# Performance work log

Hardware: AMD Instinct MI355X
Metric: run time of the kernel (lower is better)

The kernel has to match this reference:

```python
import jax, jax.numpy as jnp
import numpy as np
from jax import lax

EPS_BN = 1e-5
EPS_NORM = 1e-12
D = 6                      # max_displacement
K = 2 * D + 1              # 13

def _conv(x, w, b, stride=1, pad=0):
    out = lax.conv_general_dilated(x, w, (stride, stride), [(pad, pad), (pad, pad)],
                                   dimension_numbers=('NCHW', 'OIHW', 'NCHW'))
    return out + b[None, :, None, None]

def _bn(x, g, be):
    m = x.mean(axis=(0, 2, 3), keepdims=True)
    v = x.var(axis=(0, 2, 3), keepdims=True)  # biased var, as torch BN uses for normalization
    return g[None, :, None, None] * (x - m) * lax.rsqrt(v + EPS_BN) + be[None, :, None, None]

def _lrelu(x):
    return jax.nn.leaky_relu(x, 0.1)

def _encoder(x, w1, b1, g1, be1, w2, b2, g2, be2, w3, b3, g3, be3):
    fine = _lrelu(_bn(_conv(x, w1, b1, pad=3), g1, be1))          # (B,16,64,64)
    h = _lrelu(_bn(_conv(fine, w2, b2, stride=2, pad=2), g2, be2))  # (B,32,32,32)
    coarse = _lrelu(_bn(_conv(h, w3, b3, pad=1), g3, be3))        # (B,32,32,32)
    return coarse, fine

def _l2norm_c(f):
    n = jnp.sqrt(jnp.sum(f * f, axis=1, keepdims=True))
    return f / jnp.maximum(n, EPS_NORM)

def _correlation(fA, fB):
    # cost[b, i*K+j, h, w] = sum_c fA_n[b,c,h,w] * fB_n_pad[b,c,h+i,w+j]
    B, C, H, W = fA.shape
    fA = _l2norm_c(fA)
    fB = _l2norm_c(fB)
    fBp = jnp.pad(fB, ((0, 0), (0, 0), (D, D), (D, D)))
    costs = []
    for i in range(K):          # small fixed displacement set (169 slices)
        for j in range(K):
            costs.append(jnp.sum(fA * fBp[:, :, i:i + H, j:j + W], axis=1))
    return jnp.stack(costs, axis=1)  # (B, K*K, H, W), matches unfold ordering

def _decoder(cost, skipA, skipB, wc1, bc1, wc2, bc2, wf1, bf1, wf2, bf2, wo, bo):
    x = _lrelu(_conv(cost, wc1, bc1, pad=1))
    x = _lrelu(_conv(x, wc2, bc2, pad=1))        # (B,64,32,32)
    x = jnp.repeat(jnp.repeat(x, 2, axis=2), 2, axis=3)
    x = jnp.concatenate([x, skipA, skipB], axis=1)       # (B,96,64,64)
    x = _lrelu(_conv(x, wf1, bf1, pad=1))
    x = _lrelu(_conv(x, wf2, bf2, pad=1))        # (B,32,64,64)
    return _conv(x, wo, bo, pad=0)               # (B,2,64,64)

def setup_inputs() -> dict:
    key = jax.random.key(0)
    ks = jax.random.split(key, 16)
    B = 32
    n_disp = K * K  # 169
    f32 = jnp.float32
    w = lambda k, shp: (jax.random.normal(k, shp, dtype=f32) * 0.05)
    inp = {
        'frameA': jax.random.normal(ks[0], (B, 1, 64, 64), dtype=f32),
        'frameB': jax.random.normal(ks[1], (B, 1, 64, 64), dtype=f32),
        # shared siamese encoder params
        'w1': w(ks[2], (16, 1, 7, 7)),  'b1': jnp.zeros((16,), f32),
        'g1': jnp.ones((16,), f32),     'be1': jnp.zeros((16,), f32),
        'w2': w(ks[3], (32, 16, 5, 5)), 'b2': jnp.zeros((32,), f32),
        'g2': jnp.ones((32,), f32),     'be2': jnp.zeros((32,), f32),
        'w3': w(ks[4], (32, 32, 3, 3)), 'b3': jnp.zeros((32,), f32),
        'g3': jnp.ones((32,), f32),     'be3': jnp.zeros((32,), f32),
        # decoder params
        'wc1': w(ks[5], (128, n_disp, 3, 3)), 'bc1': jnp.zeros((128,), f32),
        'wc2': w(ks[6], (64, 128, 3, 3)),     'bc2': jnp.zeros((64,), f32),
        'wf1': w(ks[7], (64, 96, 3, 3)),      'bf1': jnp.zeros((64,), f32),
        'wf2': w(ks[8], (32, 64, 3, 3)),      'bf2': jnp.zeros((32,), f32),
        'wo':  w(ks[9], (2, 32, 1, 1)),       'bo': jnp.zeros((2,), f32),
    }
    return inp

def reference(frameA, frameB, w1, b1, g1, be1, w2, b2, g2, be2, w3, b3, g3, be3,
              wc1, bc1, wc2, bc2, wf1, bf1, wf2, bf2, wo, bo):
    coarseA, skipA = _encoder(frameA, w1, b1, g1, be1, w2, b2, g2, be2, w3, b3, g3, be3)
    coarseB, skipB = _encoder(frameB, w1, b1, g1, be1, w2, b2, g2, be2, w3, b3, g3, be3)
    cost = _correlation(coarseA, coarseB)
    return _decoder(cost, skipA, skipB, wc1, bc1, wc2, bc2, wf1, bf1, wf2, bf2, wo, bo)
```

## Files before the change

kernel.cpp:

```cpp
#include <hip/hip_runtime.h>

typedef __attribute__((ext_vector_type(4))) float f32x4;
typedef __attribute__((ext_vector_type(8))) short bf16x8;

#define BN_EPS 1e-5f
constexpr int BATCH = 32;

static inline int cdiv(int a, int b) { return (a + b - 1) / b; }

__device__ __forceinline__ float lrelu(float v) { return v > 0.f ? v : 0.1f * v; }

__device__ __forceinline__ unsigned short f2bf(float f) {
    unsigned u = __float_as_uint(f);
    u = (u + 0x7FFFu + ((u >> 16) & 1u)) >> 16;
    return (unsigned short)u;
}
__device__ __forceinline__ float bf2f(unsigned short s) {
    return __uint_as_float(((unsigned)s) << 16);
}

#define SWZ(e)  ((e) ^ ((((e) >> 6) & 3) << 3))
#define FSWZ(e) ((e) ^ ((((e) >> 5) & 7) << 2))

__global__ void prep_w_all(const float* w1, const float* w2, const float* w3, const float* w4,
                           const float* wE2s, const float* wE3s,
                           unsigned short* d1, unsigned short* d2, unsigned short* d3,
                           unsigned short* d4, unsigned short* dE2, unsigned short* dE3)
{
    int idx = blockIdx.x * blockDim.x + threadIdx.x;
    if (idx < 368640) {
        const float* src; unsigned short* dst; int COUT, CINS, CINP;
        if (idx < 221184)      { src = w1; dst = d1; COUT = 128; CINS = 169; CINP = 192; }
        else if (idx < 294912) { src = w2; dst = d2; COUT = 64;  CINS = 128; CINP = 128; idx -= 221184; }
        else if (idx < 350208) { src = w3; dst = d3; COUT = 64;  CINS = 96;  CINP = 96;  idx -= 294912; }
        else                   { src = w4; dst = d4; COUT = 32;  CINS = 64;  CINP = 64;  idx -= 350208; }
        int ic  = idx % CINP;
        int oc  = (idx / CINP) % COUT;
        int tap = idx / (CINP * COUT);
        float v = (ic < CINS) ? src[((size_t)oc * CINS + ic) * 9 + tap] : 0.f;
        dst[((size_t)tap * COUT + oc) * CINP + ic] = f2bf(v);
    } else if (idx < 381952) {
        idx -= 368640;
        int c = idx % 32, oc = (idx / 32) % 32, s = idx / 1024;
        int tap = 2 * s + (c >= 16 ? 1 : 0);
        int ic = c & 15;
        float v = (tap < 25) ? wE2s[((size_t)oc * 16 + ic) * 25 + tap] : 0.f;
        dE2[idx] = f2bf(v);
    } else if (idx < 391168) {
        idx -= 381952;
        int ic = idx % 32, oc = (idx / 32) % 32, tap = idx / 1024;
        dE3[idx] = f2bf(wE3s[((size_t)oc * 32 + ic) * 9 + tap]);
    }
}

template<int CIN, int COUT, int H, int TH, int MODE, int OM>
__global__ __launch_bounds__(256) void conv3x3_mfma(
    const unsigned short* __restrict__ in,
    const unsigned short* __restrict__ in2,
    const unsigned short* __restrict__ wT,
    const float* __restrict__ bias,
    unsigned short* __restrict__ out,
    float* __restrict__ dout,
    const float* __restrict__ w1x1,
    const float* __restrict__ b1x1)
{
    constexpr int MB = (COUT >= 64) ? 64 : COUT;
    constexpr int MFRAGS = MB / 16;
    constexpr int WM = 2;
    constexpr int MW = MFRAGS / WM;
    constexpr int NW = 4 / MW;
    constexpr int WN = TH / NW;

    __shared__ unsigned short s_w[9 * MB * 32];
    __shared__ unsigned short s_in[(TH + 2) * 18 * 32];

    const int tid  = threadIdx.x;
    const int wid  = tid >> 6;
    const int lane = tid & 63;
    const int l15  = lane & 15;
    const int kg   = lane >> 4;
    constexpr int TILESX = H / 16;
    const int bx = blockIdx.x;
    const int x0 = (bx % TILESX) * 16;
    const int y0 = (bx / TILESX) * TH;
    const int ocbase = blockIdx.y * MB;
    const int n = blockIdx.z;

    const int mw = wid % MW;
    const int nw = wid / MW;

    f32x4 acc[WM][WN];
    #pragma unroll
    for (int i = 0; i < WM; ++i) {
        #pragma unroll
        for (int r = 0; r < 4; ++r) {
            float bv = bias[ocbase + (mw * WM + i) * 16 + kg * 4 + r];
            #pragma unroll
            for (int j = 0; j < WN; ++j) acc[i][j][r] = bv;
        }
    }

    for (int c0 = 0; c0 < CIN; c0 += 32) {
        for (int t = tid; t < 9 * MB * 4; t += 256) {
            int sub = t & 3;
            int row = t >> 2;
            int tap = row / MB, oc = row % MB;
            const unsigned short* src = wT + ((size_t)(tap * COUT + ocbase + oc) * CIN + c0) + sub * 8;
            *(int4*)&s_w[SWZ(row * 32 + sub * 8)] = *(const int4*)src;
        }
        for (int t = tid; t < (TH + 2) * 18 * 4; t += 256) {
            int sub = t & 3;
            int p = t >> 2;
            int y = p / 18, x = p - y * 18;
            int gy = y0 - 1 + y, gx = x0 - 1 + x;
            int4 v = {0, 0, 0, 0};
            if ((unsigned)gy < (unsigned)H && (unsigned)gx < (unsigned)H) {
                if (MODE == 0) {
                    v = *(const int4*)&in[((size_t)(n * H + gy) * H + gx) * CIN + c0 + sub * 8];
                } else {
                    if (c0 < 64) {
                        v = *(const int4*)&in[((size_t)(n * 32 + (gy >> 1)) * 32 + (gx >> 1)) * 64 + c0 + sub * 8];
                    } else {
                        int f  = sub >> 1;
                        int cc = (sub & 1) * 8;
                        v = *(const int4*)&in2[((size_t)((f * BATCH + n) * 64 + gy) * 64 + gx) * 16 + cc];
                    }
                }
            }
            *(int4*)&s_in[SWZ(p * 32 + sub * 8)] = v;
        }
        __syncthreads();

        #pragma unroll
        for (int tap = 0; tap < 9; ++tap) {
            const int kh = tap / 3, kw = tap - (tap / 3) * 3;
            bf16x8 a[WM], b[WN];
            #pragma unroll
            for (int i = 0; i < WM; ++i) {
                int mf = mw * WM + i;
                a[i] = *(const bf16x8*)&s_w[SWZ((tap * MB + mf * 16 + l15) * 32 + kg * 8)];
            }
            #pragma unroll
            for (int j = 0; j < WN; ++j) {
                int nf = nw * WN + j;
                b[j] = *(const bf16x8*)&s_in[SWZ(((nf + kh) * 18 + l15 + kw) * 32 + kg * 8)];
            }
            #pragma unroll
            for (int i = 0; i < WM; ++i)
                #pragma unroll
                for (int j = 0; j < WN; ++j)
                    acc[i][j] = __builtin_amdgcn_mfma_f32_16x16x32_bf16(a[i], b[j], acc[i][j], 0, 0, 0);
        }
        __syncthreads();
    }

    if constexpr (OM == 2) {
        __shared__ unsigned short sC[16 * 16 * 32];
        #pragma unroll
// ... 19 lines not shown
            int c = q * 4;
            float x0v = bf2f(v.x), x1v = bf2f(v.y), x2v = bf2f(v.z), x3v = bf2f(v.w);
            a0 = fmaf(x0v, w1x1[c], a0);     a1 = fmaf(x0v, w1x1[32 + c], a1);
            a0 = fmaf(x1v, w1x1[c + 1], a0); a1 = fmaf(x1v, w1x1[32 + c + 1], a1);
            a0 = fmaf(x2v, w1x1[c + 2], a0); a1 = fmaf(x2v, w1x1[32 + c + 2], a1);
            a0 = fmaf(x3v, w1x1[c + 3], a0); a1 = fmaf(x3v, w1x1[32 + c + 3], a1);
        }
        int row = tid >> 4, col = tid & 15;
        int gy = y0 + row, gx = x0 + col;
        dout[((size_t)n * 2) * 4096 + gy * 64 + gx]     = a0;
        dout[((size_t)n * 2 + 1) * 4096 + gy * 64 + gx] = a1;
    } else {
        #pragma unroll
        for (int i = 0; i < WM; ++i) {
            int oc = ocbase + (mw * WM + i) * 16 + kg * 4;
            #pragma unroll
            for (int j = 0; j < WN; ++j) {
                int nf = nw * WN + j;
                int gy = y0 + nf, gx = x0 + l15;
                size_t base = ((size_t)(n * H + gy) * H + gx) * COUT + oc;
                if (OM == 0) {
                    ushort4 pk;
                    pk.x = f2bf(lrelu(acc[i][j][0]));
                    pk.y = f2bf(lrelu(acc[i][j][1]));
                    pk.z = f2bf(lrelu(acc[i][j][2]));
                    pk.w = f2bf(lrelu(acc[i][j][3]));
                    *(ushort4*)&out[base] = pk;
                } else {
                    *(f32x4*)&((float*)out)[base] = acc[i][j];
                }
            }
        }
    }
}

__global__ __launch_bounds__(256) void conv2s_mfma(
    const unsigned short* __restrict__ in, const unsigned short* __restrict__ wS,
    const float* __restrict__ bias, unsigned short* __restrict__ outN,
    float2* __restrict__ part)
{
    __shared__ unsigned short s_w[13 * 32 * 32];
    __shared__ unsigned short s_in[20 * 36 * 16];
    __shared__ float2 redC[4][4][8];

    const int tid = threadIdx.x;
    const int nw  = tid >> 6;
    const int lane = tid & 63;
    const int l15 = lane & 15;
    const int kg  = lane >> 4;
    const int x0 = (blockIdx.x & 1) * 16;
    const int y0 = (blockIdx.x >> 1) * 8;
    const int n  = blockIdx.z;

    f32x4 acc[2][2];
    #pragma unroll
    for (int i = 0; i < 2; ++i) {
        #pragma unroll
        for (int r = 0; r < 4; ++r) {
            float bv = bias[i * 16 + kg * 4 + r];
            acc[i][0][r] = bv; acc[i][1][r] = bv;
        }
    }

    for (int t = tid; t < 1664; t += 256) {
        int sub = t & 3, row = t >> 2;
        *(int4*)&s_w[SWZ(row * 32 + sub * 8)] = *(const int4*)&wS[row * 32 + sub * 8];
    }
    for (int t = tid; t < 1440; t += 256) {
        int sub = t & 1, p = t >> 1;
        int y = p / 36, x = p - y * 36;
        int gy = 2 * y0 - 2 + y, gx = 2 * x0 - 2 + x;
        int4 v = {0, 0, 0, 0};
        if ((unsigned)gy < 64u && (unsigned)gx < 64u)
            v = *(const int4*)&in[((size_t)(n * 64 + gy) * 64 + gx) * 16 + sub * 8];
        *(int4*)&s_in[SWZ((y * 36 + x) * 16 + sub * 8)] = v;
    }
    __syncthreads();

    #pragma unroll
    for (int s = 0; s < 13; ++s) {
        int tA = 2 * s, tB = 2 * s + 1;
        int khA = tA / 5, kwA = tA % 5;
        int khB = tB / 5, kwB = tB % 5;
        int kh = (kg < 2) ? khA : khB;
        int kw = (kg < 2) ? kwA : kwB;
        int co = (kg & 1) * 8;
        bf16x8 a[2], b[2];
        a[0] = *(const bf16x8*)&s_w[SWZ((s * 32 + l15) * 32 + kg * 8)];
        a[1] = *(const bf16x8*)&s_w[SWZ((s * 32 + 16 + l15) * 32 + kg * 8)];
        #pragma unroll
        for (int j = 0; j < 2; ++j) {
            int py = nw * 2 + j;
            b[j] = *(const bf16x8*)&s_in[SWZ(((2 * py + kh) * 36 + 2 * l15 + kw) * 16 + co)];
        }
        acc[0][0] = __builtin_amdgcn_mfma_f32_16x16x32_bf16(a[0], b[0], acc[0][0], 0, 0, 0);
        acc[0][1] = __builtin_amdgcn_mfma_f32_16x16x32_bf16(a[0], b[1], acc[0][1], 0, 0, 0);
        acc[1][0] = __builtin_amdgcn_mfma_f32_16x16x32_bf16(a[1], b[0], acc[1][0], 0, 0, 0);
        acc[1][1] = __builtin_amdgcn_mfma_f32_16x16x32_bf16(a[1], b[1], acc[1][1], 0, 0, 0);
    }

    #pragma unroll
    for (int i = 0; i < 2; ++i)
        #pragma unroll
        for (int j = 0; j < 2; ++j) {
            int gy = y0 + nw * 2 + j, gx = x0 + l15;
            ushort4 pk;
            pk.x = f2bf(acc[i][j][0]); pk.y = f2bf(acc[i][j][1]);
// ... 2 lines not shown
        }

    float t1[2][4], t2[2][4];
    #pragma unroll
    for (int i = 0; i < 2; ++i)
        #pragma unroll
        for (int r = 0; r < 4; ++r) {
            float v0 = acc[i][0][r], v1 = acc[i][1][r];
            t1[i][r] = v0 + v1;
            t2[i][r] = v0 * v0 + v1 * v1;
        }
    #pragma unroll
    for (int off = 8; off > 0; off >>= 1)
        #pragma unroll
        for (int i = 0; i < 2; ++i)
            #pragma unroll
            for (int r = 0; r < 4; ++r) {
                t1[i][r] += __shfl_down(t1[i][r], off);
                t2[i][r] += __shfl_down(t2[i][r], off);
            }
    if (l15 == 0) {
        #pragma unroll
        for (int i = 0; i < 2; ++i)
            #pragma unroll
            for (int r = 0; r < 4; ++r)
                redC[nw][kg][i * 4 + r] = make_float2(t1[i][r], t2[i][r]);
    }
    __syncthreads();
    if (tid < 32) {
        int oc = tid;
        int i = oc >> 4, kq = (oc & 15) >> 2, r = oc & 3;
        float2 s = redC[0][kq][i * 4 + r];
        #pragma unroll
        for (int w = 1; w < 4; ++w) {
            float2 p = redC[w][kq][i * 4 + r];
            s.x += p.x; s.y += p.y;
        }
        int f = n >> 5, slot = blockIdx.x * 32 + (n & 31);
        part[(size_t)(f * 32 + oc) * 256 + slot] = s;
    }
}

__global__ __launch_bounds__(256) void conv1_tiled(
    const float* __restrict__ fA, const float* __restrict__ fB,
    const float* __restrict__ w, const float* __restrict__ bias,
    unsigned short* __restrict__ outN, float2* __restrict__ part)
{
    __shared__ float s_in[38][40];
    __shared__ float s_w[49][8];
    __shared__ float2 red1[4][8];

    const int tid = threadIdx.x;
    const int tx = tid & 15, ty = tid >> 4;
    const int tile = blockIdx.x;
    const int x0 = (tile & 1) << 5;
    const int y0 = (tile >> 1) << 5;
    const int ocbase = blockIdx.y * 8;
    const int n = blockIdx.z;
    const float* in = (n < BATCH) ? (fA + (size_t)n * 4096) : (fB + (size_t)(n - BATCH) * 4096);

    for (int t = tid; t < 49 * 8; t += 256) {
        int oc = t & 7, k = t >> 3;
        s_w[k][oc] = w[(ocbase + oc) * 49 + k];
    }
    for (int t = tid; t < 38 * 38; t += 256) {
        int y = t / 38, x = t - (t / 38) * 38;
        int gy = y0 + y - 3, gx = x0 + x - 3;
        float v = 0.f;
        if ((unsigned)gy < 64u && (unsigned)gx < 64u) v = in[gy * 64 + gx];
        s_in[y][x] = v;
    }
    __syncthreads();

    float acc[8][4];
    #pragma unroll
    for (int oc = 0; oc < 8; ++oc) {
        float bv = bias[ocbase + oc];
        acc[oc][0] = bv; acc[oc][1] = bv; acc[oc][2] = bv; acc[oc][3] = bv;
    }
    #pragma unroll
    for (int kh = 0; kh < 7; ++kh) {
        #pragma unroll
        for (int kw = 0; kw < 7; ++kw) {
            float i00 = s_in[ty + kh][tx + kw];
            float i01 = s_in[ty + kh][tx + 16 + kw];
            float i10 = s_in[ty + 16 + kh][tx + kw];
            float i11 = s_in[ty + 16 + kh][tx + 16 + kw];
            #pragma unroll
            for (int oc = 0; oc < 8; ++oc) {
                float wv = s_w[kh * 7 + kw][oc];
                acc[oc][0] = fmaf(i00, wv, acc[oc][0]);
                acc[oc][1] = fmaf(i01, wv, acc[oc][1]);
                acc[oc][2] = fmaf(i10, wv, acc[oc][2]);
                acc[oc][3] = fmaf(i11, wv, acc[oc][3]);
            }
        }
    }
    #pragma unroll
    for (int i = 0; i < 2; ++i)
        #pragma unroll
        for (int j = 0; j < 2; ++j) {
            int k = i * 2 + j;
            int oy = y0 + ty + i * 16, ox = x0 + tx + j * 16;
            ushort4 p0, p1;
            p0.x = f2bf(acc[0][k]); p0.y = f2bf(acc[1][k]);
            p0.z = f2bf(acc[2][k]); p0.w = f2bf(acc[3][k]);
            p1.x = f2bf(acc[4][k]); p1.y = f2bf(acc[5][k]);
            p1.z = f2bf(acc[6][k]); p1.w = f2bf(acc[7][k]);
            unsigned short* dst = outN + ((size_t)n * 4096 + oy * 64 + ox) * 16 + ocbase;
            *(ushort4*)dst = p0;
            *(ushort4*)(dst + 4) = p1;
        }
    float v1[8], v2[8];
    #pragma unroll
    for (int oc = 0; oc < 8; ++oc) {
        v1[oc] = acc[oc][0] + acc[oc][1] + acc[oc][2] + acc[oc][3];
        v2[oc] = acc[oc][0] * acc[oc][0] + acc[oc][1] * acc[oc][1]
               + acc[oc][2] * acc[oc][2] + acc[oc][3] * acc[oc][3];
    }
    #pragma unroll
    for (int off = 32; off > 0; off >>= 1)
        #pragma unroll
        for (int oc = 0; oc < 8; ++oc) {
            v1[oc] += __shfl_down(v1[oc], off);
            v2[oc] += __shfl_down(v2[oc], off);
        }
    int wid = tid >> 6, lane = tid & 63;
    if (lane == 0)
        #pragma unroll
        for (int oc = 0; oc < 8; ++oc) red1[wid][oc] = make_float2(v1[oc], v2[oc]);
    __syncthreads();
    if (tid < 8) {
        float2 s = red1[0][tid];
        #pragma unroll
        for (int w2_ = 1; w2_ < 4; ++w2_) { s.x += red1[w2_][tid].x; s.y += red1[w2_][tid].y; }
        int f = n >> 5, slot = blockIdx.x * 32 + (n & 31);
        part[(size_t)(f * 16 + ocbase + tid) * 128 + slot] = s;
    }
}

template<int C, int NS>
__global__ void bn_part_nhwc(const float* __restrict__ x, float2* __restrict__ part, int HW)
{
    constexpr int G = 256 / C;
    int f = blockIdx.x / NS, s = blockIdx.x % NS;
    int RS = (32 * HW) / NS;
    const float* base = x + ((size_t)f * 32 * HW + (size_t)s * RS) * C;
    int c = threadIdx.x % C, rg = threadIdx.x / C;
    float s1 = 0.f, s2 = 0.f;
    for (int r = rg; r < RS; r += G) {
        float v = base[(size_t)r * C + c];
        s1 += v; s2 += v * v;
    }
    __shared__ float2 sh[256];
    sh[threadIdx.x] = make_float2(s1, s2);
    __syncthreads();
    for (int off = 128; off >= C; off >>= 1) {
        if (threadIdx.x < off) {
            float2 o = sh[threadIdx.x + off];
            sh[threadIdx.x].x += o.x; sh[threadIdx.x].y += o.y;
        }
        __syncthreads();
    }
    if (threadIdx.x < C) part[(size_t)(f * C + c) * NS + s] = sh[threadIdx.x];
}

template<int C, int NS>
__device__ __forceinline__ void finalize_stats(const float2* __restrict__ part, int f,
                                               float inv, float* sstats)
{
    __shared__ float2 red[256];
    int t = threadIdx.x;
    int c = t % C, k = t / C;
    float s1 = 0.f, s2 = 0.f;
    for (int q = k; q < NS; q += 256 / C) {
        float2 p = part[(size_t)(f * C + c) * NS + q];
        s1 += p.x; s2 += p.y;
    }
    red[t] = make_float2(s1, s2);
    __syncthreads();
    for (int off = 128; off >= C; off >>= 1) {
        if (t < off) { red[t].x += red[t + off].x; red[t].y += red[t + off].y; }
        __syncthreads();
    }
    if (t < C) {
        float m = red[t].x * inv;
        float var = red[t].y * inv - m * m;
        sstats[2 * t]     = m;
        sstats[2 * t + 1] = rsqrtf(var + BN_EPS);
    }
    __syncthreads();
}

__global__ __launch_bounds__(256) void bn1_apply(unsigned short* __restrict__ xN,
                          const float2* __restrict__ part,
                          const float* __restrict__ g, const float* __restrict__ be)
{
    __shared__ float sst[32];
    int idx = blockIdx.x * blockDim.x + threadIdx.x;
    int f = idx >> 17;
    finalize_stats<16, 128>(part, f, 1.f / (32.f * 4096.f), sst);
    unsigned short* p = xN + (size_t)idx * 16;
    int4 v0 = *(int4*)p, v1 = *(int4*)(p + 8);
    unsigned short* s = (unsigned short*)&v0;
    unsigned short o[16];
    #pragma unroll
    for (int c = 0; c < 8; ++c)
        o[c] = f2bf(lrelu((bf2f(s[c]) - sst[2 * c]) * sst[2 * c + 1] * g[c] + be[c]));
    s = (unsigned short*)&v1;
    #pragma unroll
    for (int c = 0; c < 8; ++c)
        o[8 + c] = f2bf(lrelu((bf2f(s[c]) - sst[2 * (8 + c)]) * sst[2 * (8 + c) + 1] * g[8 + c] + be[8 + c]));
    *(int4*)p       = *(int4*)&o[0];
    *(int4*)(p + 8) = *(int4*)&o[8];
}

__global__ __launch_bounds__(256) void bn2_apply(unsigned short* __restrict__ xN,
                          const float2* __restrict__ part,
                          const float* __restrict__ g, const float* __restrict__ be)
{
    __shared__ float sst[64];
    int idx = blockIdx.x * blockDim.x + threadIdx.x;
    int f = idx >> 15;
    finalize_stats<32, 256>(part, f, 1.f / (32.f * 1024.f), sst);
    unsigned short* p = xN + (size_t)idx * 32;
    unsigned short o[32];
    #pragma unroll
    for (int q = 0; q < 4; ++q) {
        int4 v = *(int4*)(p + q * 8);
        unsigned short* s = (unsigned short*)&v;
        #pragma unroll
        for (int k = 0; k < 8; ++k) {
            int c = q * 8 + k;
            o[c] = f2bf(lrelu((bf2f(s[k]) - sst[2 * c]) * sst[2 * c + 1] * g[c] + be[c]));
        }
    }
    #pragma unroll
    for (int q = 0; q < 4; ++q) *(int4*)(p + q * 8) = *(int4*)&o[q * 8];
}

__global__ __launch_bounds__(256) void bn3_l2n_nhwc(const float* __restrict__ xN,
                             const float2* __restrict__ part,
                             const float* __restrict__ g, const float* __restrict__ be,
                             float* __restrict__ outN)
{
    __shared__ float sst[64];
    int idx = blockIdx.x * blockDim.x + threadIdx.x;
    int f = idx >> 15;
    finalize_stats<32, 128>(part, f, 1.f / (32.f * 1024.f), sst);
    const float* src = xN + (size_t)idx * 32;
    float v[32];
    float ss = 0.f;
    #pragma unroll
    for (int c = 0; c < 32; ++c) {
        float t = lrelu((src[c] - sst[2 * c]) * sst[2 * c + 1] * g[c] + be[c]);
        v[c] = t; ss += t * t;
    }
    float inv = 1.f / fmaxf(sqrtf(ss), 1e-12f);
    float* dst = outN + (size_t)idx * 32;
    #pragma unroll
    for (int c = 0; c < 32; ++c) dst[c] = v[c] * inv;
}

#define CSWZ(c, w) ((c) ^ (((w) & 7) << 2))

__global__ __launch_bounds__(256) void corr_tile(const float* __restrict__ xN,
                                                 unsigned short* __restrict__ cost)
{
    __shared__ float sA[32 * 32];
    __shared__ float sB[13][32 * 32];
    __shared__ unsigned short sC[32][176];

    const int h = blockIdx.x, b = blockIdx.y;
    const float* Ab = xN + ((size_t)b * 1024 + h * 32) * 32;
    const float* Bb = xN + ((size_t)(BATCH + b) * 1024) * 32;

    {
        int t = threadIdx.x;
        int w = t >> 3, gr = t & 7;
        f32x4 v = *(const f32x4*)&Ab[w * 32 + gr * 4];
        *(f32x4*)&sA[w * 32 + CSWZ(gr * 4, w)] = v;
    }
    for (int t = threadIdx.x; t < 13 * 256; t += 256) {
        int row = t >> 8, q = t & 255;
        int w = q >> 3, gr = q & 7;
        int gh = h + row - 6;
        f32x4 v = {0.f, 0.f, 0.f, 0.f};
        if ((unsigned)gh < 32u) v = *(const f32x4*)&Bb[((size_t)gh * 32 + w) * 32 + gr * 4];
        *(f32x4*)&sB[row][w * 32 + CSWZ(gr * 4, w)] = v;
    }
    __syncthreads();

    const int w = threadIdx.x & 31;
    const int g = threadIdx.x >> 5;
    f32x4 a[8];
    #pragma unroll
    for (int gr = 0; gr < 8; ++gr) a[gr] = *(const f32x4*)&sA[w * 32 + CSWZ(gr * 4, w)];

    for (int dy = g; dy < 13; dy += 8) {
        #pragma unroll
        for (int dx = 0; dx < 13; ++dx) {
            int wb = w + dx - 6;
            float s = 0.f;
            if ((unsigned)wb < 32u) {
                #pragma unroll
                for (int gr = 0; gr < 8; ++gr) {
                    f32x4 bv = *(const f32x4*)&sB[dy][wb * 32 + CSWZ(gr * 4, wb)];
                    s += a[gr].x * bv.x + a[gr].y * bv.y + a[gr].z * bv.z + a[gr].w * bv.w;
                }
            }
            sC[w][dy * 13 + dx] = f2bf(s);
        }
    }
    __syncthreads();

    for (int t = threadIdx.x; t < 32 * 169; t += 256) {
        int ww = t / 169;
        int d  = t - ww * 169;
        cost[((size_t)(b * 1024) + h * 32 + ww) * 192 + d] = sC[ww][d];
    }
}

extern "C" void kernel_launch(void* const* d_in, const int* in_sizes, int n_in,
                              void* d_out, int out_size, void* d_ws, size_t ws_size,
                              hipStream_t stream)
{
    const float* frameA = (const float*)d_in[0];
    const float* frameB = (const float*)d_in[1];
    const float* w1  = (const float*)d_in[2];
    const float* b1  = (const float*)d_in[3];
    const float* g1  = (const float*)d_in[4];
    const float* be1 = (const float*)d_in[5];
    const float* w2  = (const float*)d_in[6];
    const float* b2  = (const float*)d_in[7];
    const float* g2  = (const float*)d_in[8];
    const float* be2 = (const float*)d_in[9];
    const float* w3  = (const float*)d_in[10];
    const float* b3  = (const float*)d_in[11];
    const float* g3  = (const float*)d_in[12];
    const float* be3 = (const float*)d_in[13];
    const float* wc1 = (const float*)d_in[14];
    const float* bc1 = (const float*)d_in[15];
    const float* wc2 = (const float*)d_in[16];
    const float* bc2 = (const float*)d_in[17];
    const float* wf1 = (const float*)d_in[18];
    const float* bf1 = (const float*)d_in[19];
    const float* wf2 = (const float*)d_in[20];
    const float* bf2 = (const float*)d_in[21];
    const float* wo  = (const float*)d_in[22];
    const float* bo  = (const float*)d_in[23];

    float* ws      = (float*)d_ws;
    float* c3N     = ws;
    float* coarseN = c3N + 2097152;
    float2* part   = (float2*)(coarseN + 2097152);
    unsigned short* fineN = (unsigned short*)(part + 16384);
    unsigned short* h2bf  = fineN + 4194304;
    unsigned short* costN = h2bf + 2097152;
    unsigned short* d1    = costN + 6291456;
    unsigned short* d2    = d1 + 4194304;
    unsigned short* f1o   = d2 + 2097152;
    unsigned short* wT1   = f1o + 8388608;
    unsigned short* wT2   = wT1 + 221184;
    unsigned short* wTf1  = wT2 + 73728;
    unsigned short* wTf2  = wTf1 + 55296;
    unsigned short* wE2   = wTf2 + 18432;
    unsigned short* wE3   = wE2 + 13312;

    const int T = 256;

    prep_w_all<<<cdiv(391168, T), T, 0, stream>>>(wc1, wc2, wf1, wf2, w2, w3,
                                                  wT1, wT2, wTf1, wTf2, wE2, wE3);

    conv1_tiled<<<dim3(4, 2, 2 * BATCH), T, 0, stream>>>(frameA, frameB, w1, b1, fineN, part);
    bn1_apply<<<1024, T, 0, stream>>>(fineN, part, g1, be1);

    conv2s_mfma<<<dim3(8, 1, 64), T, 0, stream>>>(fineN, wE2, b2, h2bf, part);
    bn2_apply<<<256, T, 0, stream>>>(h2bf, part, g2, be2);

    conv3x3_mfma<32, 32, 32, 8, 0, 1><<<dim3(8, 1, 64), T, 0, stream>>>(
        h2bf, nullptr, wE3, b3, (unsigned short*)c3N, nullptr, nullptr, nullptr);
    bn_part_nhwc<32, 128><<<2 * 128, T, 0, stream>>>(c3N, part, 1024);
    bn3_l2n_nhwc<<<256, T, 0, stream>>>(c3N, part, g3, be3, coarseN);

    corr_tile<<<dim3(32, BATCH), T, 0, stream>>>(coarseN, costN);

    conv3x3_mfma<192, 128, 32, 8, 0, 0><<<dim3(8, 2, BATCH), T, 0, stream>>>(
        costN, nullptr, wT1, bc1, d1, nullptr, nullptr, nullptr);
    conv3x3_mfma<128, 64, 32, 8, 0, 0><<<dim3(8, 1, BATCH), T, 0, stream>>>(
        d1, nullptr, wT2, bc2, d2, nullptr, nullptr, nullptr);
    conv3x3_mfma<96, 64, 64, 8, 1, 0><<<dim3(32, 1, BATCH), T, 0, stream>>>(
        d2, fineN, wTf1, bf1, f1o, nullptr, nullptr, nullptr);
    conv3x3_mfma<64, 32, 64, 16, 0, 2><<<dim3(16, 1, BATCH), T, 0, stream>>>(
        f1o, nullptr, wTf2, bf2, nullptr, (float*)d_out, wo, bo);
}
```

Measured before the change: 198.7 us.

## Fuse BN apply and L2 norm into consumer kernels, merge weight prep with conv1

Drops the separate BN apply, BN partial-stat, and BN3+L2-norm kernels. Each consumer kernel now reduces the partial statistics itself and applies BN plus leaky ReLU while loading its input tile. The conv3 epilogue emits the per-channel partial sums, and the correlation kernel computes per-pixel L2 norms in shared memory and scales the dot products by them. Weight preparation now runs as extra blocks of the conv1 kernel, removing a launch. In exchange, every block repeats the stats finalization, and the fused conv tiles recompute BN on halo reads.

Result: slower. 222.7 us (+12.1%).

```diff
diff --git a/kernel.cpp b/kernel.cpp
--- a/kernel.cpp
+++ b/kernel.cpp
@@ -21,39 +21,167 @@
 
 #define SWZ(e)  ((e) ^ ((((e) >> 6) & 3) << 3))
 #define FSWZ(e) ((e) ^ ((((e) >> 5) & 7) << 2))
-
-__global__ void prep_w_all(const float* w1, const float* w2, const float* w3, const float* w4,
-                           const float* wE2s, const float* wE3s,
-                           unsigned short* d1, unsigned short* d2, unsigned short* d3,
-                           unsigned short* d4, unsigned short* dE2, unsigned short* dE3)
+#define CSWZ(c, w) ((c) ^ (((w) & 7) << 2))
+
+template<int C, int NS>
+__device__ __forceinline__ void finalize_stats(const float2* __restrict__ part, int f,
+                                               float inv, float* sstats)
 {
-    int idx = blockIdx.x * blockDim.x + threadIdx.x;
-    if (idx < 368640) {
-        const float* src; unsigned short* dst; int COUT, CINS, CINP;
-        if (idx < 221184)      { src = w1; dst = d1; COUT = 128; CINS = 169; CINP = 192; }
-        else if (idx < 294912) { src = w2; dst = d2; COUT = 64;  CINS = 128; CINP = 128; idx -= 221184; }
-        else if (idx < 350208) { src = w3; dst = d3; COUT = 64;  CINS = 96;  CINP = 96;  idx -= 294912; }
-        else                   { src = w4; dst = d4; COUT = 32;  CINS = 64;  CINP = 64;  idx -= 350208; }
-        int ic  = idx % CINP;
-        int oc  = (idx / CINP) % COUT;
-        int tap = idx / (CINP * COUT);
-        float v = (ic < CINS) ? src[((size_t)oc * CINS + ic) * 9 + tap] : 0.f;
-        dst[((size_t)tap * COUT + oc) * CINP + ic] = f2bf(v);
-    } else if (idx < 381952) {
-        idx -= 368640;
-        int c = idx % 32, oc = (idx / 32) % 32, s = idx / 1024;
-        int tap = 2 * s + (c >= 16 ? 1 : 0);
-        int ic = c & 15;
-        float v = (tap < 25) ? wE2s[((size_t)oc * 16 + ic) * 25 + tap] : 0.f;
-        dE2[idx] = f2bf(v);
-    } else if (idx < 391168) {
-        idx -= 381952;
-        int ic = idx % 32, oc = (idx / 32) % 32, tap = idx / 1024;
-        dE3[idx] = f2bf(wE3s[((size_t)oc * 32 + ic) * 9 + tap]);
-    }
+    __shared__ float2 red[256];
+    int t = threadIdx.x;
+    int c = t % C, k = t / C;
+    float s1 = 0.f, s2 = 0.f;
+    for (int q = k; q < NS; q += 256 / C) {
+        float2 p = part[(size_t)(f * C + c) * NS + q];
+        s1 += p.x; s2 += p.y;
+    }
+    red[t] = make_float2(s1, s2);
+    __syncthreads();
+    for (int off = 128; off >= C; off >>= 1) {
+        if (t < off) { red[t].x += red[t + off].x; red[t].y += red[t + off].y; }
+        __syncthreads();
+    }
+    if (t < C) {
+        float m = red[t].x * inv;
+        float var = red[t].y * inv - m * m;
+        sstats[2 * t]     = m;
+        sstats[2 * t + 1] = rsqrtf(var + BN_EPS);
+    }
+    __syncthreads();
 }
 
-template<int CIN, int COUT, int H, int TH, int MODE, int OM>
+__global__ __launch_bounds__(256) void conv1_prep(
+    const float* __restrict__ fA, const float* __restrict__ fB,
+    const float* __restrict__ w, const float* __restrict__ bias,
+    unsigned short* __restrict__ outN, float2* __restrict__ part1,
+    const float* wd1, const float* wd2, const float* wd3, const float* wd4,
+    const float* wE2s, const float* wE3s,
+    unsigned short* d1, unsigned short* d2, unsigned short* d3,
+    unsigned short* d4, unsigned short* dE2, unsigned short* dE3)
+{
+    const int gid = blockIdx.x;
+    if (gid >= 512) {
+        int idx = (gid - 512) * 256 + threadIdx.x;
+        if (idx < 368640) {
+            const float* src; unsigned short* dst; int COUT, CINS, CINP;
+            if (idx < 221184)      { src = wd1; dst = d1; COUT = 128; CINS = 169; CINP = 192; }
+            else if (idx < 294912) { src = wd2; dst = d2; COUT = 64;  CINS = 128; CINP = 128; idx -= 221184; }
+            else if (idx < 350208) { src = wd3; dst = d3; COUT = 64;  CINS = 96;  CINP = 96;  idx -= 294912; }
+            else                   { src = wd4; dst = d4; COUT = 32;  CINS = 64;  CINP = 64;  idx -= 350208; }
+            int ic  = idx % CINP;
+            int oc  = (idx / CINP) % COUT;
+            int tap = idx / (CINP * COUT);
+            float v = (ic < CINS) ? src[((size_t)oc * CINS + ic) * 9 + tap] : 0.f;
+            dst[((size_t)tap * COUT + oc) * CINP + ic] = f2bf(v);
+        } else if (idx < 381952) {
+            idx -= 368640;
+            int c = idx % 32, oc = (idx / 32) % 32, s = idx / 1024;
+            int tap = 2 * s + (c >= 16 ? 1 : 0);
+            int ic = c & 15;
+            float v = (tap < 25) ? wE2s[((size_t)oc * 16 + ic) * 25 + tap] : 0.f;
+            dE2[idx] = f2bf(v);
+        } else if (idx < 391168) {
+            idx -= 381952;
+            int ic = idx % 32, oc = (idx / 32) % 32, tap = idx / 1024;
+            dE3[idx] = f2bf(wE3s[((size_t)oc * 32 + ic) * 9 + tap]);
+        }
+        return;
+    }
+
+    __shared__ float s_in[38][40];
+    __shared__ float s_w[49][8];
+    __shared__ float2 red1[4][8];
+
+    const int tid = threadIdx.x;
+    const int tx = tid & 15, ty = tid >> 4;
+    const int tile = gid & 3;
+    const int ocbase = ((gid >> 2) & 1) * 8;
+    const int n = gid >> 3;
+    const int x0 = (tile & 1) << 5;
+    const int y0 = (tile >> 1) << 5;
+    const float* in = (n < BATCH) ? (fA + (size_t)n * 4096) : (fB + (size_t)(n - BATCH) * 4096);
+
+    for (int t = tid; t < 49 * 8; t += 256) {
+        int oc = t & 7, k = t >> 3;
+        s_w[k][oc] = w[(ocbase + oc) * 49 + k];
+    }
+    for (int t = tid; t < 38 * 38; t += 256) {
+        int y = t / 38, x = t - (t / 38) * 38;
+        int gy = y0 + y - 3, gx = x0 + x - 3;
+        float v = 0.f;
+        if ((unsigned)gy < 64u && (unsigned)gx < 64u) v = in[gy * 64 + gx];
+        s_in[y][x] = v;
+    }
+    __syncthreads();
+
+    float acc[8][4];
+    #pragma unroll
+    for (int oc = 0; oc < 8; ++oc) {
+        float bv = bias[ocbase + oc];
+        acc[oc][0] = bv; acc[oc][1] = bv; acc[oc][2] = bv; acc[oc][3] = bv;
+    }
+    #pragma unroll
+    for (int kh = 0; kh < 7; ++kh) {
+        #pragma unroll
+        for (int kw = 0; kw < 7; ++kw) {
+            float i00 = s_in[ty + kh][tx + kw];
+            float i01 = s_in[ty + kh][tx + 16 + kw];
+            float i10 = s_in[ty + 16 + kh][tx + kw];
+            float i11 = s_in[ty + 16 + kh][tx + 16 + kw];
+            #pragma unroll
+            for (int oc = 0; oc < 8; ++oc) {
+                float wv = s_w[kh * 7 + kw][oc];
+                acc[oc][0] = fmaf(i00, wv, acc[oc][0]);
+                acc[oc][1] = fmaf(i01, wv, acc[oc][1]);
+                acc[oc][2] = fmaf(i10, wv, acc[oc][2]);
+                acc[oc][3] = fmaf(i11, wv, acc[oc][3]);
+            }
+        }
+    }
+    #pragma unroll
+    for (int i = 0; i < 2; ++i)
+        #pragma unroll
+        for (int j = 0; j < 2; ++j) {
+            int k = i * 2 + j;
+            int oy = y0 + ty + i * 16, ox = x0 + tx + j * 16;
+            ushort4 p0, p1;
+            p0.x = f2bf(acc[0][k]); p0.y = f2bf(acc[1][k]);
+            p0.z = f2bf(acc[2][k]); p0.w = f2bf(acc[3][k]);
+            p1.x = f2bf(acc[4][k]); p1.y = f2bf(acc[5][k]);
+            p1.z = f2bf(acc[6][k]); p1.w = f2bf(acc[7][k]);
+            unsigned short* dst = outN + ((size_t)n * 4096 + oy * 64 + ox) * 16 + ocbase;
+            *(ushort4*)dst = p0;
+            *(ushort4*)(dst + 4) = p1;
+        }
+    float v1[8], v2[8];
+    #pragma unroll
+    for (int oc = 0; oc < 8; ++oc) {
+        v1[oc] = acc[oc][0] + acc[oc][1] + acc[oc][2] + acc[oc][3];
+        v2[oc] = acc[oc][0] * acc[oc][0] + acc[oc][1] * acc[oc][1]
+               + acc[oc][2] * acc[oc][2] + acc[oc][3] * acc[oc][3];
+    }
+    #pragma unroll
+    for (int off = 32; off > 0; off >>= 1)
+        #pragma unroll
+        for (int oc = 0; oc < 8; ++oc) {
+            v1[oc] += __shfl_down(v1[oc], off);
+            v2[oc] += __shfl_down(v2[oc], off);
+        }
+    int wid = tid >> 6, lane = tid & 63;
+    if (lane == 0)
+        #pragma unroll
+        for (int oc = 0; oc < 8; ++oc) red1[wid][oc] = make_float2(v1[oc], v2[oc]);
+    __syncthreads();
+    if (tid < 8) {
+        float2 s = red1[0][tid];
+        #pragma unroll
+        for (int q = 1; q < 4; ++q) { s.x += red1[q][tid].x; s.y += red1[q][tid].y; }
+        int f = n >> 5, slot = tile * 32 + (n & 31);
+        part1[(size_t)(f * 16 + ocbase + tid) * 128 + slot] = s;
+    }
+}
+
+template<int CIN, int COUT, int H, int TH, int MODE, int OM, int INBN>
 __global__ __launch_bounds__(256) void conv3x3_mfma(
     const unsigned short* __restrict__ in,
     const unsigned short* __restrict__ in2,
@@ -62,7 +190,11 @@
     unsigned short* __restrict__ out,
     float* __restrict__ dout,
     const float* __restrict__ w1x1,
-    const float* __restrict__ b1x1)
+    const float* __restrict__ b1x1,
+    const float2* __restrict__ partIn,
+    const float* __restrict__ gIn,
+    const float* __restrict__ beIn,
+    float2* __restrict__ partOut)
 {
     constexpr int MB = (COUT >= 64) ? 64 : COUT;
     constexpr int MFRAGS = MB / 16;
@@ -73,6 +205,7 @@
 
     __shared__ unsigned short s_w[9 * MB * 32];
     __shared__ unsigned short s_in[(TH + 2) * 18 * 32];
+    __shared__ float sstIn[64];
 
     const int tid  = threadIdx.x;
     const int wid  = tid >> 6;
@@ -89,6 +222,11 @@
     const int mw = wid % MW;
     const int nw = wid / MW;
 
+    if constexpr (INBN == 1)
+        finalize_stats<32, 128>(partIn, 0, 1.f / (32.f * 4096.f), sstIn);
+    if constexpr (INBN == 2)
+        finalize_stats<32, 256>(partIn, n >> 5, 1.f / (32.f * 1024.f), sstIn);
+
     f32x4 acc[WM][WN];
     #pragma unroll
     for (int i = 0; i < WM; ++i) {
@@ -117,6 +255,15 @@
             if ((unsigned)gy < (unsigned)H && (unsigned)gx < (unsigned)H) {
                 if (MODE == 0) {
                     v = *(const int4*)&in[((size_t)(n * H + gy) * H + gx) * CIN + c0 + sub * 8];
+                    if constexpr (INBN == 2) {
+                        unsigned short* e = (unsigned short*)&v;
+                        #pragma unroll
+                        for (int k = 0; k < 8; ++k) {
+                            int c = c0 + sub * 8 + k;
+                            float xv = bf2f(e[k]);
+                            e[k] = f2bf(lrelu((xv - sstIn[2 * c]) * sstIn[2 * c + 1] * gIn[c] + beIn[c]));
+                        }
+                    }
                 } else {
                     if (c0 < 64) {
                         v = *(const int4*)&in[((size_t)(n * 32 + (gy >> 1)) * 32 + (gx >> 1)) * 64 + c0 + sub * 8];
@@ -124,6 +271,16 @@
                         int f  = sub >> 1;
                         int cc = (sub & 1) * 8;
                         v = *(const int4*)&in2[((size_t)((f * BATCH + n) * 64 + gy) * 64 + gx) * 16 + cc];
+                        if constexpr (INBN == 1) {
+                            unsigned short* e = (unsigned short*)&v;
+                            #pragma unroll
+                            for (int k = 0; k < 8; ++k) {
+                                int gch = f * 16 + cc + k;
+                                float xv = bf2f(e[k]);
+                                e[k] = f2bf(lrelu((xv - sstIn[2 * gch]) * sstIn[2 * gch + 1]
+                                                  * gIn[cc + k] + beIn[cc + k]));
+                            }
+                        }
                     }
                 }
             }
@@ -209,16 +366,60 @@
             }
         }
     }
+
+    if constexpr (OM == 3) {
+        __shared__ float2 redC[4][4][8];
+        float t1[2][4], t2[2][4];
+        #pragma unroll
+        for (int i = 0; i < 2; ++i)
+            #pragma unroll
+            for (int r = 0; r < 4; ++r) {
+                float v0 = acc[i][0][r], v1 = acc[i][1][r];
+                t1[i][r] = v0 + v1;
+                t2[i][r] = v0 * v0 + v1 * v1;
+            }
+        #pragma unroll
+        for (int off = 8; off > 0; off >>= 1)
+            #pragma unroll
+            for (int i = 0; i < 2; ++i)
+                #pragma unroll
+                for (int r = 0; r < 4; ++r) {
+                    t1[i][r] += __shfl_down(t1[i][r], off);
+                    t2[i][r] += __shfl_down(t2[i][r], off);
+                }
+        if (l15 == 0) {
+            #pragma unroll
+            for (int i = 0; i < 2; ++i)
+                #pragma unroll
+                for (int r = 0; r < 4; ++r)
+                    redC[nw][kg][i * 4 + r] = make_float2(t1[i][r], t2[i][r]);
+        }
+        __syncthreads();
+        if (tid < 32) {
+            int oc = tid;
+            int i = oc >> 4, kq = (oc & 15) >> 2, r = oc & 3;
+            float2 s = redC[0][kq][i * 4 + r];
+            #pragma unroll
+            for (int q = 1; q < 4; ++q) {
+                float2 p = redC[q][kq][i * 4 + r];
+                s.x += p.x; s.y += p.y;
+            }
+            int f = n >> 5, slot = bx * 32 + (n & 31);
+            partOut[(size_t)(f * 32 + oc) * 256 + slot] = s;
+        }
+    }
 }
 
 __global__ __launch_bounds__(256) void conv2s_mfma(
     const unsigned short* __restrict__ in, const unsigned short* __restrict__ wS,
     const float* __restrict__ bias, unsigned short* __restrict__ outN,
-    float2* __restrict__ part)
+    const float2* __restrict__ part1, const float* __restrict__ g1,
+    const float* __restrict__ be1, float2* __restrict__ part2)
 {
     __shared__ unsigned short s_w[13 * 32 * 32];
     __shared__ unsigned short s_in[20 * 36 * 16];
     __shared__ float2 redC[4][4][8];
+    __shared__ float sst[32];
 
     const int tid = threadIdx.x;
     const int nw  = tid >> 6;
@@ -229,6 +430,8 @@
     const int y0 = (blockIdx.x >> 1) * 8;
     const int n  = blockIdx.z;
 
+    finalize_stats<16, 128>(part1, n >> 5, 1.f / (32.f * 4096.f), sst);
+
     f32x4 acc[2][2];
     #pragma unroll
     for (int i = 0; i < 2; ++i) {
@@ -248,8 +451,16 @@
         int y = p / 36, x = p - y * 36;
         int gy = 2 * y0 - 2 + y, gx = 2 * x0 - 2 + x;
         int4 v = {0, 0, 0, 0};
-        if ((unsigned)gy < 64u && (unsigned)gx < 64u)
+        if ((unsigned)gy < 64u && (unsigned)gx < 64u) {
             v = *(const int4*)&in[((size_t)(n * 64 + gy) * 64 + gx) * 16 + sub * 8];
+            unsigned short* e = (unsigned short*)&v;
+            #pragma unroll
+            for (int k = 0; k < 8; ++k) {
+                int c = sub * 8 + k;
+                float xv = bf2f(e[k]);
+                e[k] = f2bf(lrelu((xv - sst[2 * c]) * sst[2 * c + 1] * g1[c] + be1[c]));
+            }
+        }
         *(int4*)&s_in[SWZ((y * 36 + x) * 16 + sub * 8)] = v;
     }
     __syncthreads();
@@ -318,246 +529,32 @@
         int i = oc >> 4, kq = (oc & 15) >> 2, r = oc & 3;
         float2 s = redC[0][kq][i * 4 + r];
         #pragma unroll
-        for (int w = 1; w < 4; ++w) {
-            float2 p = redC[w][kq][i * 4 + r];
+        for (int q = 1; q < 4; ++q) {
+            float2 p = redC[q][kq][i * 4 + r];
             s.x += p.x; s.y += p.y;
         }
         int f = n >> 5, slot = blockIdx.x * 32 + (n & 31);
-        part[(size_t)(f * 32 + oc) * 256 + slot] = s;
+        part2[(size_t)(f * 32 + oc) * 256 + slot] = s;
     }
 }
 
-__global__ __launch_bounds__(256) void conv1_tiled(
-    const float* __restrict__ fA, const float* __restrict__ fB,
-    const float* __restrict__ w, const float* __restrict__ bias,
-    unsigned short* __restrict__ outN, float2* __restrict__ part)
-{
-    __shared__ float s_in[38][40];
-    __shared__ float s_w[49][8];
-    __shared__ float2 red1[4][8];
-
-    const int tid = threadIdx.x;
-    const int tx = tid & 15, ty = tid >> 4;
-    const int tile = blockIdx.x;
-    const int x0 = (tile & 1) << 5;
-    const int y0 = (tile >> 1) << 5;
-    const int ocbase = blockIdx.y * 8;
-    const int n = blockIdx.z;
-    const float* in = (n < BATCH) ? (fA + (size_t)n * 4096) : (fB + (size_t)(n - BATCH) * 4096);
-
-    for (int t = tid; t < 49 * 8; t += 256) {
-        int oc = t & 7, k = t >> 3;
-        s_w[k][oc] = w[(ocbase + oc) * 49 + k];
-    }
-    for (int t = tid; t < 38 * 38; t += 256) {
-        int y = t / 38, x = t - (t / 38) * 38;
-        int gy = y0 + y - 3, gx = x0 + x - 3;
-        float v = 0.f;
-        if ((unsigned)gy < 64u && (unsigned)gx < 64u) v = in[gy * 64 + gx];
-        s_in[y][x] = v;
-    }
-    __syncthreads();
-
-    float acc[8][4];
-    #pragma unroll
-    for (int oc = 0; oc < 8; ++oc) {
-        float bv = bias[ocbase + oc];
-        acc[oc][0] = bv; acc[oc][1] = bv; acc[oc][2] = bv; acc[oc][3] = bv;
-    }
-    #pragma unroll
-    for (int kh = 0; kh < 7; ++kh) {
-        #pragma unroll
-        for (int kw = 0; kw < 7; ++kw) {
-            float i00 = s_in[ty + kh][tx + kw];
-            float i01 = s_in[ty + kh][tx + 16 + kw];
-            float i10 = s_in[ty + 16 + kh][tx + kw];
-            float i11 = s_in[ty + 16 + kh][tx + 16 + kw];
-            #pragma unroll
-            for (int oc = 0; oc < 8; ++oc) {
-                float wv = s_w[kh * 7 + kw][oc];
-                acc[oc][0] = fmaf(i00, wv, acc[oc][0]);
-                acc[oc][1] = fmaf(i01, wv, acc[oc][1]);
-                acc[oc][2] = fmaf(i10, wv, acc[oc][2]);
-                acc[oc][3] = fmaf(i11, wv, acc[oc][3]);
-            }
-        }
-    }
-    #pragma unroll
-    for (int i = 0; i < 2; ++i)
-        #pragma unroll
-        for (int j = 0; j < 2; ++j) {
-            int k = i * 2 + j;
-            int oy = y0 + ty + i * 16, ox = x0 + tx + j * 16;
-            ushort4 p0, p1;
-            p0.x = f2bf(acc[0][k]); p0.y = f2bf(acc[1][k]);
-            p0.z = f2bf(acc[2][k]); p0.w = f2bf(acc[3][k]);
-            p1.x = f2bf(acc[4][k]); p1.y = f2bf(acc[5][k]);
-            p1.z = f2bf(acc[6][k]); p1.w = f2bf(acc[7][k]);
-            unsigned short* dst = outN + ((size_t)n * 4096 + oy * 64 + ox) * 16 + ocbase;
-            *(ushort4*)dst = p0;
-            *(ushort4*)(dst + 4) = p1;
-        }
-    float v1[8], v2[8];
-    #pragma unroll
-    for (int oc = 0; oc < 8; ++oc) {
-        v1[oc] = acc[oc][0] + acc[oc][1] + acc[oc][2] + acc[oc][3];
-        v2[oc] = acc[oc][0] * acc[oc][0] + acc[oc][1] * acc[oc][1]
-               + acc[oc][2] * acc[oc][2] + acc[oc][3] * acc[oc][3];
-    }
-    #pragma unroll
-    for (int off = 32; off > 0; off >>= 1)
-        #pragma unroll
-        for (int oc = 0; oc < 8; ++oc) {
-            v1[oc] += __shfl_down(v1[oc], off);
-            v2[oc] += __shfl_down(v2[oc], off);
-        }
-    int wid = tid >> 6, lane = tid & 63;
-    if (lane == 0)
-        #pragma unroll
-        for (int oc = 0; oc < 8; ++oc) red1[wid][oc] = make_float2(v1[oc], v2[oc]);
-    __syncthreads();
-    if (tid < 8) {
-        float2 s = red1[0][tid];
-        #pragma unroll
-        for (int w2_ = 1; w2_ < 4; ++w2_) { s.x += red1[w2_][tid].x; s.y += red1[w2_][tid].y; }
-        int f = n >> 5, slot = blockIdx.x * 32 + (n & 31);
-        part[(size_t)(f * 16 + ocbase + tid) * 128 + slot] = s;
-    }
-}
-
-template<int C, int NS>
-__global__ void bn_part_nhwc(const float* __restrict__ x, float2* __restrict__ part, int HW)
-{
-    constexpr int G = 256 / C;
-    int f = blockIdx.x / NS, s = blockIdx.x % NS;
-    int RS = (32 * HW) / NS;
-    const float* base = x + ((size_t)f * 32 * HW + (size_t)s * RS) * C;
-    int c = threadIdx.x % C, rg = threadIdx.x / C;
-    float s1 = 0.f, s2 = 0.f;
-    for (int r = rg; r < RS; r += G) {
-        float v = base[(size_t)r * C + c];
-        s1 += v; s2 += v * v;
-    }
-    __shared__ float2 sh[256];
-    sh[threadIdx.x] = make_float2(s1, s2);
-    __syncthreads();
-    for (int off = 128; off >= C; off >>= 1) {
-        if (threadIdx.x < off) {
-            float2 o = sh[threadIdx.x + off];
-            sh[threadIdx.x].x += o.x; sh[threadIdx.x].y += o.y;
-        }
-        __syncthreads();
-    }
-    if (threadIdx.x < C) part[(size_t)(f * C + c) * NS + s] = sh[threadIdx.x];
-}
-
-template<int C, int NS>
-__device__ __forceinline__ void finalize_stats(const float2* __restrict__ part, int f,
-                                               float inv, float* sstats)
-{
-    __shared__ float2 red[256];
-    int t = threadIdx.x;
-    int c = t % C, k = t / C;
-    float s1 = 0.f, s2 = 0.f;
-    for (int q = k; q < NS; q += 256 / C) {
-        float2 p = part[(size_t)(f * C + c) * NS + q];
-        s1 += p.x; s2 += p.y;
-    }
-    red[t] = make_float2(s1, s2);
-    __syncthreads();
-    for (int off = 128; off >= C; off >>= 1) {
-        if (t < off) { red[t].x += red[t + off].x; red[t].y += red[t + off].y; }
-        __syncthreads();
-    }
-    if (t < C) {
-        float m = red[t].x * inv;
-        float var = red[t].y * inv - m * m;
-        sstats[2 * t]     = m;
-        sstats[2 * t + 1] = rsqrtf(var + BN_EPS);
-    }
-    __syncthreads();
-}
-
-__global__ __launch_bounds__(256) void bn1_apply(unsigned short* __restrict__ xN,
-                          const float2* __restrict__ part,
-                          const float* __restrict__ g, const float* __restrict__ be)
-{
-    __shared__ float sst[32];
-    int idx = blockIdx.x * blockDim.x + threadIdx.x;
-    int f = idx >> 17;
-    finalize_stats<16, 128>(part, f, 1.f / (32.f * 4096.f), sst);
-    unsigned short* p = xN + (size_t)idx * 16;
-    int4 v0 = *(int4*)p, v1 = *(int4*)(p + 8);
-    unsigned short* s = (unsigned short*)&v0;
-    unsigned short o[16];
-    #pragma unroll
-    for (int c = 0; c < 8; ++c)
-        o[c] = f2bf(lrelu((bf2f(s[c]) - sst[2 * c]) * sst[2 * c + 1] * g[c] + be[c]));
-    s = (unsigned short*)&v1;
-    #pragma unroll
-    for (int c = 0; c < 8; ++c)
-        o[8 + c] = f2bf(lrelu((bf2f(s[c]) - sst[2 * (8 + c)]) * sst[2 * (8 + c) + 1] * g[8 + c] + be[8 + c]));
-    *(int4*)p       = *(int4*)&o[0];
-    *(int4*)(p + 8) = *(int4*)&o[8];
-}
-
-__global__ __launch_bounds__(256) void bn2_apply(unsigned short* __restrict__ xN,
-                          const float2* __restrict__ part,
-                          const float* __restrict__ g, const float* __restrict__ be)
-{
-    __shared__ float sst[64];
-    int idx = blockIdx.x * blockDim.x + threadIdx.x;
-    int f = idx >> 15;
-    finalize_stats<32, 256>(part, f, 1.f / (32.f * 1024.f), sst);
-    unsigned short* p = xN + (size_t)idx * 32;
-    unsigned short o[32];
-    #pragma unroll
-    for (int q = 0; q < 4; ++q) {
-        int4 v = *(int4*)(p + q * 8);
-        unsigned short* s = (unsigned short*)&v;
-        #pragma unroll
-        for (int k = 0; k < 8; ++k) {
-            int c = q * 8 + k;
-            o[c] = f2bf(lrelu((bf2f(s[k]) - sst[2 * c]) * sst[2 * c + 1] * g[c] + be[c]));
-        }
-    }
-    #pragma unroll
-    for (int q = 0; q < 4; ++q) *(int4*)(p + q * 8) = *(int4*)&o[q * 8];
-}
-
-__global__ __launch_bounds__(256) void bn3_l2n_nhwc(const float* __restrict__ xN,
-                             const float2* __restrict__ part,
-                             const float* __restrict__ g, const float* __restrict__ be,
-                             float* __restrict__ outN)
-{
-    __shared__ float sst[64];
-    int idx = blockIdx.x * blockDim.x + threadIdx.x;
-    int f = idx >> 15;
-    finalize_stats<32, 128>(part, f, 1.f / (32.f * 1024.f), sst);
-    const float* src = xN + (size_t)idx * 32;
-    float v[32];
-    float ss = 0.f;
-    #pragma unroll
-    for (int c = 0; c < 32; ++c) {
-        float t = lrelu((src[c] - sst[2 * c]) * sst[2 * c + 1] * g[c] + be[c]);
-        v[c] = t; ss += t * t;
-    }
-    float inv = 1.f / fmaxf(sqrtf(ss), 1e-12f);
-    float* dst = outN + (size_t)idx * 32;
-    #pragma unroll
-    for (int c = 0; c < 32; ++c) dst[c] = v[c] * inv;
-}
-
-#define CSWZ(c, w) ((c) ^ (((w) & 7) << 2))
-
 __global__ __launch_bounds__(256) void corr_tile(const float* __restrict__ xN,
+                                                 const float2* __restrict__ part3,
+                                                 const float* __restrict__ g,
+                                                 const float* __restrict__ be,
                                                  unsigned short* __restrict__ cost)
 {
     __shared__ float sA[32 * 32];
     __shared__ float sB[13][32 * 32];
     __shared__ unsigned short sC[32][176];
+    __shared__ float sst0[64], sst1[64];
+    __shared__ float rnA[32], rnB[13][32];
 
     const int h = blockIdx.x, b = blockIdx.y;
+    const float inv = 1.f / (32.f * 1024.f);
+    finalize_stats<32, 256>(part3, 0, inv, sst0);
+    finalize_stats<32, 256>(part3, 1, inv, sst1);
+
     const float* Ab = xN + ((size_t)b * 1024 + h * 32) * 32;
     const float* Bb = xN + ((size_t)(BATCH + b) * 1024) * 32;
 
@@ -565,6 +562,11 @@
         int t = threadIdx.x;
         int w = t >> 3, gr = t & 7;
         f32x4 v = *(const f32x4*)&Ab[w * 32 + gr * 4];
+        #pragma unroll
+        for (int k = 0; k < 4; ++k) {
+            int c = gr * 4 + k;
+            v[k] = lrelu((v[k] - sst0[2 * c]) * sst0[2 * c + 1] * g[c] + be[c]);
+        }
         *(f32x4*)&sA[w * 32 + CSWZ(gr * 4, w)] = v;
     }
     for (int t = threadIdx.x; t < 13 * 256; t += 256) {
@@ -572,18 +574,48 @@
         int w = q >> 3, gr = q & 7;
         int gh = h + row - 6;
         f32x4 v = {0.f, 0.f, 0.f, 0.f};
-        if ((unsigned)gh < 32u) v = *(const f32x4*)&Bb[((size_t)gh * 32 + w) * 32 + gr * 4];
+        if ((unsigned)gh < 32u) {
+            v = *(const f32x4*)&Bb[((size_t)gh * 32 + w) * 32 + gr * 4];
+            #pragma unroll
+            for (int k = 0; k < 4; ++k) {
+                int c = gr * 4 + k;
+                v[k] = lrelu((v[k] - sst1[2 * c]) * sst1[2 * c + 1] * g[c] + be[c]);
+            }
+        }
         *(f32x4*)&sB[row][w * 32 + CSWZ(gr * 4, w)] = v;
     }
     __syncthreads();
 
+    for (int t = threadIdx.x; t < 448; t += 256) {
+        float ss = 0.f;
+        if (t < 32) {
+            #pragma unroll
+            for (int gr = 0; gr < 8; ++gr) {
+                f32x4 v = *(const f32x4*)&sA[t * 32 + CSWZ(gr * 4, t)];
+                ss += v.x * v.x + v.y * v.y + v.z * v.z + v.w * v.w;
+            }
+            rnA[t] = 1.f / fmaxf(sqrtf(ss), 1e-12f);
+        } else {
+            int idx = t - 32;
+            int dy = idx >> 5, wc = idx & 31;
+            #pragma unroll
+            for (int gr = 0; gr < 8; ++gr) {
+                f32x4 v = *(const f32x4*)&sB[dy][wc * 32 + CSWZ(gr * 4, wc)];
+                ss += v.x * v.x + v.y * v.y + v.z * v.z + v.w * v.w;
+            }
+            rnB[dy][wc] = 1.f / fmaxf(sqrtf(ss), 1e-12f);
+        }
+    }
+    __syncthreads();
+
     const int w = threadIdx.x & 31;
-    const int g = threadIdx.x >> 5;
+    const int gq = threadIdx.x >> 5;
     f32x4 a[8];
     #pragma unroll
     for (int gr = 0; gr < 8; ++gr) a[gr] = *(const f32x4*)&sA[w * 32 + CSWZ(gr * 4, w)];
-
-    for (int dy = g; dy < 13; dy += 8) {
+    float rna = rnA[w];
+
+    for (int dy = gq; dy < 13; dy += 8) {
         #pragma unroll
         for (int dx = 0; dx < 13; ++dx) {
             int wb = w + dx - 6;
@@ -594,6 +626,7 @@
                     f32x4 bv = *(const f32x4*)&sB[dy][wb * 32 + CSWZ(gr * 4, wb)];
                     s += a[gr].x * bv.x + a[gr].y * bv.y + a[gr].z * bv.z + a[gr].w * bv.w;
                 }
+                s *= rna * rnB[dy][wb];
             }
             sC[w][dy * 13 + dx] = f2bf(s);
         }
@@ -638,9 +671,10 @@
 
     float* ws      = (float*)d_ws;
     float* c3N     = ws;
-    float* coarseN = c3N + 2097152;
-    float2* part   = (float2*)(coarseN + 2097152);
-    unsigned short* fineN = (unsigned short*)(part + 16384);
+    float2* part1  = (float2*)(c3N + 2097152);
+    float2* part2  = part1 + 4096;
+    float2* part3  = part2 + 16384;
+    unsigned short* fineN = (unsigned short*)(part3 + 16384);
     unsigned short* h2bf  = fineN + 4194304;
     unsigned short* costN = h2bf + 2097152;
     unsigned short* d1    = costN + 6291456;
@@ -655,28 +689,29 @@
 
     const int T = 256;
 
-    prep_w_all<<<cdiv(391168, T), T, 0, stream>>>(wc1, wc2, wf1, wf2, w2, w3,
-                                                  wT1, wT2, wTf1, wTf2, wE2, wE3);
-
-    conv1_tiled<<<dim3(4, 2, 2 * BATCH), T, 0, stream>>>(frameA, frameB, w1, b1, fineN, part);
-    bn1_apply<<<1024, T, 0, stream>>>(fineN, part, g1, be1);
-
-    conv2s_mfma<<<dim3(8, 1, 64), T, 0, stream>>>(fineN, wE2, b2, h2bf, part);
-    bn2_apply<<<256, T, 0, stream>>>(h2bf, part, g2, be2);
-
-    conv3x3_mfma<32, 32, 32, 8, 0, 1><<<dim3(8, 1, 64), T, 0, stream>>>(
-        h2bf, nullptr, wE3, b3, (unsigned short*)c3N, nullptr, nullptr, nullptr);
-    bn_part_nhwc<32, 128><<<2 * 128, T, 0, stream>>>(c3N, part, 1024);
-    bn3_l2n_nhwc<<<256, T, 0, stream>>>(c3N, part, g3, be3, coarseN);
-
-    corr_tile<<<dim3(32, BATCH), T, 0, stream>>>(coarseN, costN);
-
-    conv3x3_mfma<192, 128, 32, 8, 0, 0><<<dim3(8, 2, BATCH), T, 0, stream>>>(
-        costN, nullptr, wT1, bc1, d1, nullptr, nullptr, nullptr);
-    conv3x3_mfma<128, 64, 32, 8, 0, 0><<<dim3(8, 1, BATCH), T, 0, stream>>>(
-        d1, nullptr, wT2, bc2, d2, nullptr, nullptr, nullptr);
-    conv3x3_mfma<96, 64, 64, 8, 1, 0><<<dim3(32, 1, BATCH), T, 0, stream>>>(
-        d2, fineN, wTf1, bf1, f1o, nullptr, nullptr, nullptr);
-    conv3x3_mfma<64, 32, 64, 16, 0, 2><<<dim3(16, 1, BATCH), T, 0, stream>>>(
-        f1o, nullptr, wTf2, bf2, nullptr, (float*)d_out, wo, bo);
+    conv1_prep<<<2040, T, 0, stream>>>(frameA, frameB, w1, b1, fineN, part1,
+                                       wc1, wc2, wf1, wf2, w2, w3,
+                                       wT1, wT2, wTf1, wTf2, wE2, wE3);
+
+    conv2s_mfma<<<dim3(8, 1, 64), T, 0, stream>>>(fineN, wE2, b2, h2bf,
+                                                  part1, g1, be1, part2);
+
+    conv3x3_mfma<32, 32, 32, 8, 0, 3, 2><<<dim3(8, 1, 64), T, 0, stream>>>(
+        h2bf, nullptr, wE3, b3, (unsigned short*)c3N, nullptr, nullptr, nullptr,
+        part2, g2, be2, part3);
+
+    corr_tile<<<dim3(32, BATCH), T, 0, stream>>>(c3N, part3, g3, be3, costN);
+
+    conv3x3_mfma<192, 128, 32, 8, 0, 0, 0><<<dim3(8, 2, BATCH), T, 0, stream>>>(
+        costN, nullptr, wT1, bc1, d1, nullptr, nullptr, nullptr,
+        nullptr, nullptr, nullptr, nullptr);
+    conv3x3_mfma<128, 64, 32, 8, 0, 0, 0><<<dim3(8, 1, BATCH), T, 0, stream>>>(
+        d1, nullptr, wT2, bc2, d2, nullptr, nullptr, nullptr,
+        nullptr, nullptr, nullptr, nullptr);
+    conv3x3_mfma<96, 64, 64, 8, 1, 0, 1><<<dim3(32, 1, BATCH), T, 0, stream>>>(
+        d2, fineN, wTf1, bf1, f1o, nullptr, nullptr, nullptr,
+        part1, g1, be1, nullptr);
+    conv3x3_mfma<64, 32, 64, 16, 0, 2, 0><<<dim3(16, 1, BATCH), T, 0, stream>>>(
+        f1o, nullptr, wTf2, bf2, nullptr, (float*)d_out, wo, bo,
+        nullptr, nullptr, nullptr, nullptr);
 }
```
